# Performance work log

Measured on AMD Instinct MI355X. Metric: run time of the kernel, lower is better.

Reference implementation:

```python
import jax, jax.numpy as jnp
import numpy as np

EPS = 1e-5
DN = ('NCHW', 'OIHW', 'NCHW')

def conv3(x, w):
    return jax.lax.conv_general_dilated(x, w, (1, 1), 'SAME', dimension_numbers=DN)

def conv1(x, w, b):
    # w: [O, I]
    return jnp.einsum('oi,bihw->bohw', w, x) + b[None, :, None, None]

def bn_relu(x, p):
    # p: [4, C] rows = scale, bias, mean, var (eval-mode BatchNorm2d)
    s, b, m, v = p[0], p[1], p[2], p[3]
    y = s[None, :, None, None] * (x - m[None, :, None, None]) * jax.lax.rsqrt(v[None, :, None, None] + EPS) + b[None, :, None, None]
    return jax.nn.relu(y)

def setup_inputs() -> dict:
    key = jax.random.key(0)
    ks = jax.random.split(key, 24)
    B, Cin, H, W = 2, 2048, 60, 60
    Ci = Cin // 4            # 512 inter_channels
    Cq = Ci // 8             # 64  query/key channels
    Co = 40                  # out_channels (classes)
    f32 = jnp.float32
    def bn(C):
        return jnp.stack([jnp.ones((C,), f32), jnp.zeros((C,), f32), jnp.zeros((C,), f32), jnp.ones((C,), f32)])
    s3 = 1.0 / np.sqrt(9 * Ci)
    inp = {
        'x': jax.random.normal(ks[0], (B, Cin, H, W), f32),
        'd': jax.random.uniform(ks[1], (B, 1, H, W), f32),
        'w_s0': jax.random.normal(ks[2], (Ci, Cin, 3, 3), f32) * (1.0 / np.sqrt(9 * Cin)),
        'bn_s0': bn(Ci),
        'wq': jax.random.normal(ks[3], (Cq, Ci), f32) * (1.0 / np.sqrt(Ci)),
        'bq': jnp.zeros((Cq,), f32),
        'wk': jax.random.normal(ks[4], (Cq, Ci), f32) * (1.0 / np.sqrt(Ci)),
        'bk': jnp.zeros((Cq,), f32),
        'wv': jax.random.normal(ks[5], (Ci, Ci), f32) * (1.0 / np.sqrt(Ci)),
        'bv': jnp.zeros((Ci,), f32),
        'gamma_sa': jnp.zeros((), f32) + 0.5,   # nonzero so attention branch contributes
        'lamb': jnp.zeros((), f32) + 0.3,
        'w_s1': jax.random.normal(ks[6], (Ci, Ci, 3, 3), f32) * s3,
        'bn_s1': bn(Ci),
        'w6': jax.random.normal(ks[7], (Co, Ci), f32) * (1.0 / np.sqrt(Ci)),
        'b6': jnp.zeros((Co,), f32),
        'w_c0': jax.random.normal(ks[8], (Ci, Cin, 3, 3), f32) * (1.0 / np.sqrt(9 * Cin)),
        'bn_c0': bn(Ci),
        'gamma_sc': jnp.zeros((), f32) + 0.5,
        'w_c1': jax.random.normal(ks[9], (Ci, Ci, 3, 3), f32) * s3,
        'bn_c1': bn(Ci),
        'w7': jax.random.normal(ks[10], (Co, Ci), f32) * (1.0 / np.sqrt(Ci)),
        'b7': jnp.zeros((Co,), f32),
        'w8': jax.random.normal(ks[11], (Co, Ci), f32) * (1.0 / np.sqrt(Ci)),
        'b8': jnp.zeros((Co,), f32),
    }
    return inp

def reference(x, d, w_s0, bn_s0, wq, bq, wk, bk, wv, bv, gamma_sa, lamb,
              w_s1, bn_s1, w6, b6, w_c0, bn_c0, gamma_sc, w_c1, bn_c1, w7, b7, w8, b8):
    B, _, H, W = x.shape
    N = H * W
    # ---- position-attention (PAM_Module_Dep, fuse_type='a', depth_order=2) branch ----
    feat1 = bn_relu(conv3(x, w_s0), bn_s0)               # [B, Ci, H, W]
    Ci = feat1.shape[1]
    q = conv1(feat1, wq, bq).reshape(B, -1, N)           # [B, Cq, N]
    k = conv1(feat1, wk, bk).reshape(B, -1, N)           # [B, Cq, N]
    v = conv1(feat1, wv, bv).reshape(B, Ci, N)           # [B, Ci, N]
    energy = jnp.einsum('bcn,bcm->bnm', q, k)            # [B, N, N], n=query pixel
    df = d.reshape(B, N)
    dd = (df[:, :, None] - df[:, None, :]) ** 2          # depth_order == 2
    attention = jax.nn.softmax(energy + lamb * dd, axis=-1)
    sa = jnp.einsum('bcm,bnm->bcn', v, attention).reshape(B, Ci, H, W)
    sa = gamma_sa * sa + feat1
    sa_conv = bn_relu(conv3(sa, w_s1), bn_s1)            # post_conv=True
    sa_output = conv1(sa_conv, w6, b6)                   # Dropout2d is identity in eval
    # ---- channel-attention (CAM_Module) branch ----
    feat2 = bn_relu(conv3(x, w_c0), bn_c0)               # [B, Ci, H, W]
    xf = feat2.reshape(B, Ci, N)
    cen = jnp.einsum('bcn,bdn->bcd', xf, xf)             # [B, Ci, Ci]
    cen = jnp.max(cen, axis=-1, keepdims=True) - cen
    catt = jax.nn.softmax(cen, axis=-1)
    sc = jnp.einsum('bcd,bdn->bcn', catt, xf).reshape(B, Ci, H, W)
    sc = gamma_sc * sc + feat2
    sc_conv = bn_relu(conv3(sc, w_c1), bn_c1)
    sc_output = conv1(sc_conv, w7, b7)
    # ---- fusion head ----
    feat_sum = sa_conv + sc_conv
    sasc_output = conv1(feat_sum, w8, b8)
    return (sasc_output, sa_output, sc_output)
```

## Files before the change

kernel.cpp:

```cpp
#include <hip/hip_runtime.h>
#include <stdint.h>

#define DI __device__ __forceinline__

typedef unsigned short u16;
typedef unsigned int u32;
typedef __attribute__((ext_vector_type(8))) short short8;
typedef __attribute__((ext_vector_type(4))) float floatx4;

constexpr int NPIX = 3600;
constexpr int NK   = 3712;
constexpr int PP   = 4096;
constexpr int GUARD= 128;
constexpr int CIN  = 2048, CI = 512, CQ = 64;

constexpr size_t OFF_XPM    = 0;
constexpr size_t OFF_SAF    = 0;
constexpr size_t OFF_PBUF   = 14745600;
constexpr size_t OFF_SACONV = 0;
constexpr size_t OFF_SCCONV = 8388608;
constexpr size_t R1_END     = 42812416;
constexpr size_t OFF_FEAT1  = R1_END;
constexpr size_t OFF_FEAT2  = OFF_FEAT1 + 8388608;
constexpr size_t OFF_SAPM   = OFF_FEAT2 + 8388608;
constexpr size_t OFF_SCPM   = OFF_SAPM + 8912896;
constexpr size_t OFF_W      = OFF_SCPM + 8912896;
constexpr size_t OFF_WQB = OFF_W;
constexpr size_t OFF_WKB = OFF_W + 65536;
constexpr size_t OFF_WVB = OFF_W + 131072;
constexpr size_t OFF_QC  = OFF_W + 655360;
constexpr size_t OFF_KC  = OFF_W + 1576960;
constexpr size_t OFF_VC  = OFF_W + 2498560;
constexpr size_t OFF_WT1 = OFF_W;
constexpr size_t OFF_WT2 = OFF_W + 4718592;
constexpr size_t OFF_VCM = OFF_W + 9871360;
constexpr size_t OFF_CEN = OFF_W + 17473536;
constexpr size_t OFF_CATT= OFF_W + 19570688;
constexpr size_t OFF_WH  = OFF_W + 20619264;
constexpr size_t WS_NEED = OFF_W + 37748736;

DI float b2f(u16 s){ u32 u = ((u32)s)<<16; float f; __builtin_memcpy(&f,&u,4); return f; }
DI u16 f2b(float f){ u32 u; __builtin_memcpy(&u,&f,4); u32 r=(u+0x7fffu+((u>>16)&1u))>>16; return (u16)r; }
DI int pad_of(int n){ int y=n/60, x=n-y*60; return ((y+2)<<6)+x+2; }
DI bool interior(int p){ int py=p>>6, px=p&63; return (py>=2)&&(py<62)&&(px>=2)&&(px<62); }
DI int compact_of(int p){ return ((p>>6)-2)*60 + (p&63) - 2; }
DI void gll16(const void* g, void* l){
  __builtin_amdgcn_global_load_lds((const __attribute__((address_space(1))) void*)g,
                                   (__attribute__((address_space(3))) void*)l, 16, 0, 0);
}
DI float wred_min(float v){
#pragma unroll
  for(int m=32;m;m>>=1) v=fminf(v,__shfl_xor(v,m,64));
  return v;
}
DI float wred_sum(float v){
#pragma unroll
  for(int m=32;m;m>>=1) v+=__shfl_xor(v,m,64);
  return v;
}

struct GArgs {
  const u16 *A, *A2, *B, *B2; u16 *Cb, *Cb2, *Cb3; float* Cf;
  const u16* resid;
  const float *bn, *bn2, *bias, *bias2, *bias3, *gamma, *lambp, *dR, *dC;
  long sA, sB, sC, sres;
  int M, N, KT, ktps, lda, ldb, ldc, Mclamp, Nclamp, nsplit, ksplit, kps;
};

template<int MODE, bool SHIFT, bool NCAT, bool DUALZ, int U, bool SPLITK, bool KCAT2=false>
__global__ __launch_bounds__(256) void k_gemm(GArgs g){
  __shared__ alignas(16) short As[U*4096];
  __shared__ alignas(16) short Bs[U*4096];
  const int bz = blockIdx.z;
  const int sel = DUALZ ? (bz>>1) : 0;
  int bt  = DUALZ ? (bz&1)  : bz;
  int slice = 0;
  if constexpr(SPLITK){ bt = bz / g.ksplit; slice = bz - bt*g.ksplit; }
  const u16* Ab = ((DUALZ && sel) ? g.A2 : g.A) + (long)bt*g.sA;
  const u16* Ab2 = KCAT2 ? (g.A2 + (long)bt*g.sA) : nullptr;
  const u16* Bb = ((DUALZ && sel) ? g.B2 : g.B) + (long)bt*g.sB;
  const int m0 = blockIdx.x*128, n0 = blockIdx.y*128;
  const int tid = threadIdx.x, wid = tid>>6, lane = tid&63;
  const int wr = wid>>1, wc = wid&1;
  const int fr = lane&15, fq = lane>>4;
  const int srow = lane>>2;
  const int swz = ((lane&3) ^ ((lane>>3)&3)) << 3;

  long raB[2], rbB[2];
#pragma unroll
  for(int h=0;h<2;h++){
    long ra = m0 + wid*32 + h*16 + srow;
    if (!SHIFT) ra = (ra > g.Mclamp) ? (long)g.Mclamp : ra;
    raB[h] = ra*(long)g.lda + swz;
    long rb = n0 + wid*32 + h*16 + srow;
    rb = (rb > g.Nclamp) ? (long)g.Nclamp : rb;
    rbB[h] = rb*(long)g.ldb + swz;
  }
  const int ldsOff[2] = { (wid*32)*64, (wid*32+16)*64 };
  const int rswz = (fq ^ ((fr>>1)&3)) << 3;
  const int aRdO = (wr*64+fr)*32 + rswz;
  const int bRdO = (wc*64+fr)*32 + rswz;

  floatx4 acc[4][4];
#pragma unroll
  for(int i=0;i<4;i++)
#pragma unroll
    for(int j=0;j<4;j++)
#pragma unroll
      for(int e=0;e<4;e++) acc[i][j][e]=0.f;

  if constexpr(SHIFT){
    const int KB = g.ktps;
    for(int s=0; s<9; ++s){
      const long aoff = (long)((s/3)*64 + (s-(s/3)*3) - 65)*g.lda;
      const long boff = (long)s*KB*32;
      for(int kb=0; kb<KB; kb+=U){
        __syncthreads();
#pragma unroll
        for(int u=0;u<U;++u){
          const int ko = (kb+u)*32;
#pragma unroll
          for(int h=0;h<2;h++){
            gll16(Ab + raB[h] + aoff + ko, (char*)As + u*8192 + ldsOff[h]);
            gll16(Bb + rbB[h] + boff + ko, (char*)Bs + u*8192 + ldsOff[h]);
          }
        }
        __syncthreads();
#pragma unroll
        for(int u=0;u<U;++u){
          short8 af[4], bfv[4];
#pragma unroll
          for(int mi=0;mi<4;mi++) af[mi]  = *(const short8*)(As + u*4096 + aRdO + mi*512);
#pragma unroll
          for(int ni=0;ni<4;ni++) bfv[ni] = *(const short8*)(Bs + u*4096 + bRdO + ni*512);
#pragma unroll
          for(int mi=0;mi<4;mi++)
#pragma unroll
            for(int ni=0;ni<4;ni++)
              acc[mi][ni] = __builtin_amdgcn_mfma_f32_16x16x32_bf16(af[mi], bfv[ni], acc[mi][ni], 0,0,0);
        }
      }
    }
  } else {
    int kt0 = 0, ktN = g.KT;
    if constexpr(SPLITK){ kt0 = slice*g.kps; ktN = min(g.KT, kt0+g.kps); }
    for(int kt=kt0; kt<ktN; kt+=U){
      __syncthreads();
#pragma unroll
      for(int u=0;u<U;++u){
        if (kt+u < ktN){
          int ko = kt+u;
          const u16* srcA = Ab;
          if constexpr(KCAT2){ if (ko >= (g.KT>>1)){ srcA = Ab2; ko -= (g.KT>>1); } }
          const int koB = (kt+u)*32;
#pragma unroll
          for(int h=0;h<2;h++){
            gll16(srcA + raB[h] + ko*32, (char*)As + u*8192 + ldsOff[h]);
            gll16(Bb + rbB[h] + koB, (char*)Bs + u*8192 + ldsOff[h]);
          }
        }
      }
      __syncthreads();
#pragma unroll
      for(int u=0;u<U;++u){
        if (kt+u < ktN){
          short8 af[4], bfv[4];
#pragma unroll
          for(int mi=0;mi<4;mi++) af[mi]  = *(const short8*)(As + u*4096 + aRdO + mi*512);
#pragma unroll
          for(int ni=0;ni<4;ni++) bfv[ni] = *(const short8*)(Bs + u*4096 + bRdO + ni*512);
#pragma unroll
          for(int mi=0;mi<4;mi++)
#pragma unroll
            for(int ni=0;ni<4;ni++)
              acc[mi][ni] = __builtin_amdgcn_mfma_f32_16x16x32_bf16(af[mi], bfv[ni], acc[mi][ni], 0,0,0);
        }
      }
    }
  }

  float* Cf = (MODE==3) ? g.Cf + (long)bt*g.sC : nullptr;
  const u16* Rb = (MODE==5) ? g.resid + (long)bt*g.sres : nullptr;
  float gamv=0.f;
  if constexpr(MODE==5) gamv = *g.gamma;

#pragma unroll
  for(int ni=0;ni<4;ni++){
    const int gc = n0 + wc*64 + ni*16 + fr;
    if (gc >= g.N) continue;
    if constexpr(MODE==0){
      const float* bnP = g.bn; u16* CbP = g.Cb; int oc = gc;
      if constexpr(DUALZ){ if (sel){ bnP = g.bn2; CbP = g.Cb2; } }
      if constexpr(NCAT){ if (gc >= g.nsplit){ bnP = g.bn2; CbP = g.Cb2; oc = gc - g.nsplit; } }
      CbP += (long)bt*g.sC;
      const float s_=bnP[oc], bb=bnP[CI+oc], mm=bnP[2*CI+oc], vv=bnP[3*CI+oc];
      const float cA = s_*rsqrtf(vv+1e-5f), cB = bb - cA*mm;
#pragma unroll
      for(int mi=0;mi<4;mi++)
#pragma unroll
        for(int j=0;j<4;j++){
          const int gr = m0 + wr*64 + mi*16 + fq*4 + j;
          if (interior(gr)) CbP[(size_t)gr*g.ldc + oc] = f2b(fmaxf(cA*acc[mi][ni][j]+cB, 0.f));
        }
    } else if constexpr(MODE==6){
      u16* dst; int col, ld; float bs;
      if (gc < 64){ dst = g.Cb  + (long)bt*((long)NPIX*CQ); col=gc;     ld=CQ; bs=g.bias[gc]; }
      else if (gc < 128){ dst = g.Cb2 + (long)bt*((long)NPIX*CQ); col=gc-64; ld=CQ; bs=g.bias2[gc-64]; }
      else { dst = g.Cb3 + (long)bt*((long)NPIX*CI); col=gc-128; ld=CI; bs=g.bias3[gc-128]; }
#pragma unroll
      for(int mi=0;mi<4;mi++)
#pragma unroll
        for(int j=0;j<4;j++){
          const int gr = m0 + wr*64 + mi*16 + fq*4 + j;
          if (interior(gr)) dst[(size_t)compact_of(gr)*ld + col] = f2b(acc[mi][ni][j] + bs);
        }
    } else if constexpr(MODE==3){
#pragma unroll
      for(int mi=0;mi<4;mi++)
#pragma unroll
        for(int j=0;j<4;j++){
          const int gr = m0 + wr*64 + mi*16 + fq*4 + j;
          if (gr < g.M){
            if constexpr(SPLITK) atomicAdd(&Cf[(size_t)gr*g.ldc + gc], acc[mi][ni][j]);
            else Cf[(size_t)gr*g.ldc + gc] = acc[mi][ni][j];
          }
        }
    } else if constexpr(MODE==5){
      u16* CbP = g.Cb + (long)bt*g.sC;
#pragma unroll
      for(int mi=0;mi<4;mi++)
#pragma unroll
        for(int j=0;j<4;j++){
          const int gr = m0 + wr*64 + mi*16 + fq*4 + j;
          if (interior(gr)){ const size_t o=(size_t)gr*g.ldc + gc; CbP[o] = f2b(gamv*acc[mi][ni][j] + b2f(Rb[o])); }
        }
    } else if constexpr(MODE==7){
      size_t hb; int oc; const float* bp;
      if (gc < 40){ hb = 0; oc = gc; bp = g.bias; }
      else if (gc < 80){ hb = 288000; oc = gc-40; bp = g.bias2; }
      else { hb = 576000; oc = gc-80; bp = g.bias3; }
      float* dst = g.Cf + hb + (size_t)bt*144000 + (size_t)oc*3600;
      const float bsv = bp[oc];
#pragma unroll
      for(int mi=0;mi<4;mi++)
#pragma unroll
        for(int j=0;j<4;j++){
          const int gr = m0 + wr*64 + mi*16 + fq*4 + j;
          if (interior(gr)) dst[compact_of(gr)] = acc[mi][ni][j] + bsv;
        }
    }
  }
}

__global__ __launch_bounds__(512) void k_esm(const u16* __restrict__ qc, const u16* __restrict__ kc,
    const float* __restrict__ dd, const float* __restrict__ lamp, u16* __restrict__ pb){
  __shared__ float lm[8][16], ll[8][16];
  const int tid = threadIdx.x, wave = tid>>6, lane = tid&63;
  const int fr = lane&15, fq = lane>>4;
  const int q0 = blockIdx.x*16;
  const float lam = *lamp;
  const u16* qp = qc + (size_t)(q0+fr)*CQ + fq*8;
  const short8 qa0 = *(const short8*)(qp);
  const short8 qa1 = *(const short8*)(qp + 32);
  float dr[4];
#pragma unroll
  for(int j=0;j<4;j++) dr[j] = dd[q0 + fq*4 + j];
  float m[4], l[4];
#pragma unroll
  for(int j=0;j<4;j++){ m[j] = -3e38f; l[j] = 0.f; }

  for(int t=wave; t<29; t+=8){
    const int n0 = t*128;
    floatx4 s[8]; float dc[8];
#pragma unroll
    for(int ni=0; ni<8; ++ni){
      const int ccol = min(n0 + ni*16 + fr, NPIX-1);
      const u16* kp = kc + (size_t)ccol*CQ + fq*8;
      const short8 b0 = *(const short8*)(kp);
      const short8 b1 = *(const short8*)(kp + 32);
      floatx4 z = {0.f,0.f,0.f,0.f};
      z = __builtin_amdgcn_mfma_f32_16x16x32_bf16(qa0, b0, z, 0,0,0);
      s[ni] = __builtin_amdgcn_mfma_f32_16x16x32_bf16(qa1, b1, z, 0,0,0);
      dc[ni] = dd[ccol];
    }
#pragma unroll
    for(int j=0;j<4;j++){
      float vals[8]; float tmax = -3e38f;
#pragma unroll
      for(int ni=0;ni<8;ni++){
        const float td = dr[j] - dc[ni];
        float v = s[ni][j] + lam*td*td;
        if (n0 + ni*16 + fr >= NPIX) v = -3e38f;
        vals[ni] = v; tmax = fmaxf(tmax, v);
      }
      tmax = fmaxf(tmax, __shfl_xor(tmax,1,64));
      tmax = fmaxf(tmax, __shfl_xor(tmax,2,64));
      tmax = fmaxf(tmax, __shfl_xor(tmax,4,64));
      tmax = fmaxf(tmax, __shfl_xor(tmax,8,64));
      const float mn = fmaxf(m[j], tmax);
      float ts = 0.f;
#pragma unroll
      for(int ni=0;ni<8;ni++) ts += __expf(vals[ni]-mn);
      ts += __shfl_xor(ts,1,64);
      ts += __shfl_xor(ts,2,64);
      ts += __shfl_xor(ts,4,64);
      ts += __shfl_xor(ts,8,64);
      l[j] = l[j]*__expf(m[j]-mn) + ts;
      m[j] = mn;
    }
  }
  if (fr == 0){
#pragma unroll
    for(int j=0;j<4;j++){ lm[wave][fq*4+j] = m[j]; ll[wave][fq*4+j] = l[j]; }
  }
  __syncthreads();
  float M[4], L[4];
#pragma unroll
  for(int j=0;j<4;j++){
    const int row = fq*4 + j;
    float mm = lm[0][row];
#pragma unroll
    for(int w=1;w<8;w++) mm = fmaxf(mm, lm[w][row]);
    float ss = 0.f;
#pragma unroll
    for(int w=0;w<8;w++) ss += ll[w][row]*__expf(lm[w][row]-mm);
    M[j] = mm; L[j] = 1.f/ss;
  }

  for(int t=wave; t<29; t+=8){
    const int n0 = t*128;
#pragma unroll
    for(int ni=0; ni<8; ++ni){
      const int col = n0 + ni*16 + fr;
      const int ccol = min(col, NPIX-1);
      const u16* kp = kc + (size_t)ccol*CQ + fq*8;
      const short8 b0 = *(const short8*)(kp);
      const short8 b1 = *(const short8*)(kp + 32);
      floatx4 z = {0.f,0.f,0.f,0.f};
      z = __builtin_amdgcn_mfma_f32_16x16x32_bf16(qa0, b0, z, 0,0,0);
      const floatx4 sv = __builtin_amdgcn_mfma_f32_16x16x32_bf16(qa1, b1, z, 0,0,0);
      const float dcv = dd[ccol];
#pragma unroll
      for(int j=0;j<4;j++){
        const int q = q0 + fq*4 + j;
        const float td = dr[j] - dcv;
        float v = sv[j] + lam*td*td;
        if (col >= NPIX) v = -3e38f;
        const float p = __expf(v - M[j])*L[j];
        pb[(size_t)q*NK + col] = f2b(p);
      }
    }
  }
}

__global__ __launch_bounds__(256) void k_padx(const float* __restrict__ x, u16* __restrict__ xpm){
  __shared__ alignas(16) u16 t[64][72];
  const int n0 = blockIdx.x*64, c0 = blockIdx.y*64, b = blockIdx.z;
  const float* xb = x + (size_t)b*CIN*NPIX;
  u16* ob = xpm + (size_t)b*(PP+2*GUARD)*CIN + (size_t)GUARD*CIN;
  const int tid = threadIdx.x;
#pragma unroll
  for(int pass=0; pass<2; ++pass){
    const int cl = pass*32 + (tid>>3);
    const int nn = (tid&7)*8;
    const int n = n0 + nn;
    const float* src = xb + (size_t)(c0+cl)*NPIX + n;
    u16 r[8];
    if (n + 7 < NPIX){
      const float4 v0 = *(const float4*)src;
      const float4 v1 = *(const float4*)(src+4);
      r[0]=f2b(v0.x); r[1]=f2b(v0.y); r[2]=f2b(v0.z); r[3]=f2b(v0.w);
      r[4]=f2b(v1.x); r[5]=f2b(v1.y); r[6]=f2b(v1.z); r[7]=f2b(v1.w);
    } else {
#pragma unroll
      for(int j=0;j<8;j++){ const int nj=n+j; r[j] = (nj<NPIX)? f2b(src[j]) : (u16)0; }
    }
    __builtin_memcpy(&t[cl][nn], r, 16);
  }
  __syncthreads();
#pragma unroll
  for(int pass=0; pass<2; ++pass){
    const int nl = pass*32 + (tid>>3);
    const int cc = (tid&7)*8;
    const int n = n0 + nl;
    if (n < NPIX){
      u16 v[8];
#pragma unroll
      for(int j=0;j<8;j++) v[j] = t[cc+j][nl];
      uint4 vv; __builtin_memcpy(&vv, v, 16);
      *(uint4*)(ob + (size_t)pad_of(n)*CIN + c0 + cc) = vv;
    }
  }
}

template<bool PADIN>
__global__ __launch_bounds__(256) void k_to_cm(const u16* __restrict__ in, u16* __restrict__ out,
                                               long sIn, long sOut){
  __shared__ alignas(16) u16 t[64][72];
  const int n0 = blockIdx.x*64, c0 = blockIdx.y*64, b = blockIdx.z;
  const u16* ib = in + (size_t)b*sIn;
  u16* ob = out + (size_t)b*sOut;
  const int tid = threadIdx.x;
#pragma unroll
  for(int pass=0; pass<2; ++pass){
    const int nl = pass*32 + (tid>>3);
    const int cc = (tid&7)*8;
    const int n = n0 + nl;
    uint4 v = {0,0,0,0};
    if (n < NPIX){
      const int r = PADIN ? pad_of(n) : n;
      v = *(const uint4*)(ib + (size_t)r*CI + c0 + cc);
    }
    *(uint4*)&t[nl][cc] = v;
  }
  __syncthreads();
#pragma unroll
  for(int pass=0; pass<2; ++pass){
    const int cl = pass*32 + (tid>>3);
    const int nn = (tid&7)*8;
    const int n = n0 + nn;
    if (n < NK){
      u16 v[8];
#pragma unroll
      for(int j=0;j<8;j++) v[j] = t[nn+j][cl];
      uint4 vv; __builtin_memcpy(&vv, v, 16);
      *(uint4*)(ob + (size_t)(c0+cl)*NK + n) = vv;
    }
  }
}

__global__ __launch_bounds__(256) void k_wt(const float* __restrict__ w, u16* __restrict__ wt, int Kc){
  const int idx = blockIdx.x*256 + threadIdx.x;
  const int o = idx / Kc, i = idx - o*Kc;
  u16 v[9];
#pragma unroll
  for(int s=0;s<9;s++) v[s] = f2b(w[(size_t)idx*9 + s]);
#pragma unroll
  for(int s=0;s<9;s++) wt[(size_t)o*9*Kc + (size_t)s*Kc + i] = v[s];
}

__global__ __launch_bounds__(256) void k_cvt(const float* __restrict__ src, u16* __restrict__ dst, int n){
  const int i = blockIdx.x*256 + threadIdx.x;
  if (i < n) dst[i] = f2b(src[i]);
}

__global__ __launch_bounds__(256) void k_whead(const float* __restrict__ w6, const float* __restrict__ w7,
                                               const float* __restrict__ w8, u16* __restrict__ wh){
  const int idx = blockIdx.x*256 + threadIdx.x;
  const int r = idx >> 10, k = idx & 1023;
  float v = 0.f;
  if (r < 40) v = w8[r*512 + (k & 511)];
  else if (r < 80){ if (k < 512) v = w6[(r-40)*512 + k]; }
  else { if (k >= 512) v = w7[(r-80)*512 + (k-512)]; }
  wh[idx] = f2b(v);
}

__global__ __launch_bounds__(256) void k_csoftmax(const float* __restrict__ cen, u16* __restrict__ catt){
  const int c = blockIdx.x, b = blockIdx.y, tid = threadIdx.x;
  const float* e = cen + ((size_t)b*CI + c)*CI;
  u16* o = catt + ((size_t)b*CI + c)*CI;
  __shared__ float red[8];
  const float a0 = e[tid], a1 = e[tid+256];
  float lmin = fminf(a0,a1);
  lmin = wred_min(lmin);
  if((tid&63)==0) red[tid>>6]=lmin;
  __syncthreads();
  const float m0 = fminf(fminf(red[0],red[1]),fminf(red[2],red[3]));
  const float x0 = __expf(m0-a0), x1 = __expf(m0-a1);
  float ls = x0+x1;
  ls = wred_sum(ls);
  if((tid&63)==0) red[4+(tid>>6)]=ls;
  __syncthreads();
  const float inv = 1.f/(red[4]+red[5]+red[6]+red[7]);
  o[tid] = f2b(x0*inv); o[tid+256] = f2b(x1*inv);
}

__global__ __launch_bounds__(256) void k_pv_ep(const float* __restrict__ saf, const u16* __restrict__ f1,
                                               u16* __restrict__ sapm, const float* __restrict__ gamma){
  const int idx = blockIdx.x*256 + threadIdx.x;
  const int n = idx >> 6, c = (idx & 63) * 8;
  const float gam = *gamma;
  const int p = pad_of(n);
  const float4 v0 = *(const float4*)(saf + (size_t)n*CI + c);
  const float4 v1 = *(const float4*)(saf + (size_t)n*CI + c + 4);
  const uint4 rv = *(const uint4*)(f1 + (size_t)p*CI + c);
  const u16* rp = (const u16*)&rv;
  u16 o[8];
  o[0]=f2b(gam*v0.x + b2f(rp[0])); o[1]=f2b(gam*v0.y + b2f(rp[1]));
  o[2]=f2b(gam*v0.z + b2f(rp[2])); o[3]=f2b(gam*v0.w + b2f(rp[3]));
  o[4]=f2b(gam*v1.x + b2f(rp[4])); o[5]=f2b(gam*v1.y + b2f(rp[5]));
  o[6]=f2b(gam*v1.z + b2f(rp[6])); o[7]=f2b(gam*v1.w + b2f(rp[7]));
  uint4 ov; __builtin_memcpy(&ov, o, 16);
  *(uint4*)(sapm + (size_t)p*CI + c) = ov;
}

extern "C" void kernel_launch(void* const* d_in, const int* in_sizes, int n_in,
                              void* d_out, int out_size, void* d_ws, size_t ws_size,
                              hipStream_t stream){
  (void)in_sizes; (void)n_in; (void)out_size;
  if (ws_size < WS_NEED) return;

  const float* x    = (const float*)d_in[0];
  const float* dd   = (const float*)d_in[1];
  const float* w_s0 = (const float*)d_in[2];
  const float* bn_s0= (const float*)d_in[3];
  const float* wq   = (const float*)d_in[4];
  const float* bq   = (const float*)d_in[5];
  const float* wk   = (const float*)d_in[6];
  const float* bk   = (const float*)d_in[7];
  const float* wv   = (const float*)d_in[8];
  const float* bv   = (const float*)d_in[9];
  const float* gsa  = (const float*)d_in[10];
  const float* lam  = (const float*)d_in[11];
  const float* w_s1 = (const float*)d_in[12];
  const float* bn_s1= (const float*)d_in[13];
  const float* w6   = (const float*)d_in[14];
  const float* b6   = (const float*)d_in[15];
  const float* w_c0 = (const float*)d_in[16];
  const float* bn_c0= (const float*)d_in[17];
  const float* gsc  = (const float*)d_in[18];
  const float* w_c1 = (const float*)d_in[19];
  const float* bn_c1= (const float*)d_in[20];
  const float* w7   = (const float*)d_in[21];
  const float* b7   = (const float*)d_in[22];
  const float* w8   = (const float*)d_in[23];
  const float* b8   = (const float*)d_in[24];

  char* W = (char*)d_ws;
  u16*   XPM   = (u16*)(W + OFF_XPM);
  float* SAF   = (float*)(W + OFF_SAF);
  u16*   PB    = (u16*)(W + OFF_PBUF);
  u16*   SACONV= (u16*)(W + OFF_SACONV);
  u16*   SCCONV= (u16*)(W + OFF_SCCONV);
  u16*   F1    = (u16*)(W + OFF_FEAT1);
  u16*   F2    = (u16*)(W + OFF_FEAT2);
  u16*   SAPM  = (u16*)(W + OFF_SAPM);
  u16*   SCPM  = (u16*)(W + OFF_SCPM);
  u16*   WTT   = (u16*)(W + OFF_W);
  u16*   WQB   = (u16*)(W + OFF_WQB);
  u16*   WKB   = (u16*)(W + OFF_WKB);
  u16*   WVB   = (u16*)(W + OFF_WVB);
  u16*   QC    = (u16*)(W + OFF_QC);
  u16*   KC    = (u16*)(W + OFF_KC);
  u16*   VC    = (u16*)(W + OFF_VC);
  u16*   WT1   = (u16*)(W + OFF_WT1);
  u16*   WT2   = (u16*)(W + OFF_WT2);
  u16*   WH    = (u16*)(W + OFF_WH);
  u16*   VCM   = (u16*)(W + OFF_VCM);
  u16*   F2CM  = VCM;
  float* CEN   = (float*)(W + OFF_CEN);
  u16*   CATT  = (u16*)(W + OFF_CATT);
  float* OUT   = (float*)d_out;

  hipMemsetAsync(XPM,  0, (size_t)2*(PP+2*GUARD)*CIN*2, stream);
  hipMemsetAsync(SAPM, 0, (size_t)2*(PP+2*GUARD)*CI*2,  stream);
  hipMemsetAsync(SCPM, 0, (size_t)2*(PP+2*GUARD)*CI*2,  stream);

  k_padx<<<dim3(57,32,2),256,0,stream>>>(x, XPM);

  k_wt<<<(512*2048)/256,256,0,stream>>>(w_s0, WTT, 2048);
  k_wt<<<(512*2048)/256,256,0,stream>>>(w_c0, WTT + (size_t)512*9*2048, 2048);
  GArgs a{};
  a.A = XPM + (size_t)GUARD*CIN; a.B = WTT; a.Cb = F1; a.Cb2 = F2;
  a.bn = bn_s0; a.bn2 = bn_c0;
  a.sA = (long)(PP+2*GUARD)*CIN; a.sB = 0; a.sC = (long)PP*CI;
  a.M = PP; a.N = 1024; a.nsplit = 512; a.KT = 576; a.ktps = 64;
  a.lda = CIN; a.ldb = 9*2048; a.ldc = CI; a.Mclamp = PP-1; a.Nclamp = 1023;
  k_gemm<0,true,true,false,4,false><<<dim3(32,8,2),256,0,stream>>>(a);

  k_cvt<<<(64*512+255)/256,256,0,stream>>>(wq, WQB, 64*512);
  k_cvt<<<(64*512+255)/256,256,0,stream>>>(wk, WKB, 64*512);
  k_cvt<<<(512*512+255)/256,256,0,stream>>>(wv, WVB, 512*512);

  GArgs q{};
  q.A = F1; q.sA = (long)PP*CI; q.lda = CI;
  q.M = PP; q.Mclamp = PP-1; q.KT = 16; q.ktps = 16;
  q.B = WQB; q.sB = 0; q.ldb = CI; q.N = 640; q.Nclamp = 639;
  q.Cb = QC; q.Cb2 = KC; q.Cb3 = VC; q.bias = bq; q.bias2 = bk; q.bias3 = bv;
  k_gemm<6,false,false,false,4,false><<<dim3(32,5,2),256,0,stream>>>(q);

  k_to_cm<false><<<dim3(NK/64, CI/64, 2),256,0,stream>>>(VC, VCM, (long)NPIX*CI, (long)CI*NK);

  for(int bb=0; bb<2; ++bb){
    k_esm<<<dim3(225),512,0,stream>>>(QC + (size_t)bb*NPIX*CQ, KC + (size_t)bb*NPIX*CQ,
                                      dd + (size_t)bb*NPIX, lam, PB);
    hipMemsetAsync(SAF, 0, (size_t)NPIX*CI*4, stream);
    GArgs p{};
    p.A = PB; p.B = VCM + (size_t)bb*CI*NK;
    p.Cf = SAF;
    p.M = NPIX; p.N = CI; p.KT = NK/32; p.ktps = NK/32;
    p.lda = NK; p.ldb = NK; p.ldc = CI; p.sC = 0;
    p.Mclamp = NPIX-1; p.Nclamp = CI-1;
    p.ksplit = 2; p.kps = NK/64;
    k_gemm<3,false,false,false,4,true><<<dim3(29, 4, 2),256,0,stream>>>(p);
    k_pv_ep<<<dim3(NPIX*CI/8/256),256,0,stream>>>(SAF, F1 + (size_t)bb*PP*CI,
                                                  SAPM + (size_t)bb*(PP+2*GUARD)*CI + (size_t)GUARD*CI, gsa);
  }

  k_to_cm<true><<<dim3(NK/64, CI/64, 2),256,0,stream>>>(F2, F2CM, (long)PP*CI, (long)CI*NK);
  hipMemsetAsync(CEN, 0, (size_t)2*CI*CI*4, stream);
  GArgs c{};
  c.A = F2CM; c.B = F2CM; c.Cf = CEN;
  c.sA = (long)CI*NK; c.sB = (long)CI*NK; c.sC = (long)CI*CI;
  c.M = CI; c.N = CI; c.KT = NK/32; c.ktps = NK/32;
  c.lda = NK; c.ldb = NK; c.ldc = CI; c.Mclamp = CI-1; c.Nclamp = CI-1;
  c.ksplit = 8; c.kps = (NK/32 + 7)/8;
  k_gemm<3,false,false,false,1,true><<<dim3(4, 4, 16),256,0,stream>>>(c);
  k_csoftmax<<<dim3(CI,2),256,0,stream>>>(CEN, CATT);
  GArgs s{};
  s.A = F2; s.B = CATT;
  s.Cb = SCPM + (size_t)GUARD*CI;
  s.resid = F2; s.gamma = gsc;
  s.sA = (long)PP*CI; s.sB = (long)CI*CI; s.sC = (long)(PP+2*GUARD)*CI; s.sres = (long)PP*CI;
  s.M = PP; s.N = CI; s.KT = 16; s.ktps = 16;
  s.lda = CI; s.ldb = CI; s.ldc = CI; s.Mclamp = PP-1; s.Nclamp = CI-1;
  k_gemm<5,false,false,false,4,false><<<dim3(32, 4, 2),256,0,stream>>>(s);

  k_wt<<<(512*512)/256,256,0,stream>>>(w_s1, WT1, 512);
  k_wt<<<(512*512)/256,256,0,stream>>>(w_c1, WT2, 512);
  k_whead<<<dim3(120*1024/256),256,0,stream>>>(w6, w7, w8, WH);
  GArgs t{};
  t.A = SAPM + (size_t)GUARD*CI; t.A2 = SCPM + (size_t)GUARD*CI;
  t.B = WT1; t.B2 = WT2;
  t.Cb = SACONV; t.Cb2 = SCCONV; t.bn = bn_s1; t.bn2 = bn_c1;
  t.sA = (long)(PP+2*GUARD)*CI; t.sB = 0; t.sC = (long)PP*CI;
  t.M = PP; t.N = CI; t.KT = 144; t.ktps = 16;
  t.lda = CI; t.ldb = 9*512; t.ldc = CI; t.Mclamp = PP-1; t.Nclamp = CI-1;
  k_gemm<0,true,false,true,4,false><<<dim3(32,4,4),256,0,stream>>>(t);

  GArgs h{};
  h.A = SACONV; h.A2 = SCCONV; h.B = WH; h.Cf = OUT;
  h.bias = b8; h.bias2 = b6; h.bias3 = b7;
  h.sA = (long)PP*CI; h.sB = 0; h.sC = 0;
  h.M = PP; h.N = 120; h.KT = 32; h.ktps = 32;
  h.lda = CI; h.ldb = 1024; h.ldc = 0; h.Mclamp = PP-1; h.Nclamp = 119;
  k_gemm<7,false,false,false,4,false,true><<<dim3(32,1,2),256,0,stream>>>(h);
}
```

Measured before the change: 752.9 us.

## Skip padded border tiles, zero only halo rows, merge weight-conversion launches

```diff
diff --git a/kernel.cpp b/kernel.cpp
--- a/kernel.cpp
+++ b/kernel.cpp
@@ -64,7 +64,7 @@
   const u16* resid;
   const float *bn, *bn2, *bias, *bias2, *bias3, *gamma, *lambp, *dR, *dC;
   long sA, sB, sC, sres;
-  int M, N, KT, ktps, lda, ldb, ldc, Mclamp, Nclamp, nsplit, ksplit, kps;
+  int M, N, KT, ktps, lda, ldb, ldc, Mclamp, Nclamp, nsplit, ksplit, kps, moff;
 };
 
 template<int MODE, bool SHIFT, bool NCAT, bool DUALZ, int U, bool SPLITK, bool KCAT2=false>
@@ -79,7 +79,7 @@
   const u16* Ab = ((DUALZ && sel) ? g.A2 : g.A) + (long)bt*g.sA;
   const u16* Ab2 = KCAT2 ? (g.A2 + (long)bt*g.sA) : nullptr;
   const u16* Bb = ((DUALZ && sel) ? g.B2 : g.B) + (long)bt*g.sB;
-  const int m0 = blockIdx.x*128, n0 = blockIdx.y*128;
+  const int m0 = blockIdx.x*128 + g.moff, n0 = blockIdx.y*128;
   const int tid = threadIdx.x, wid = tid>>6, lane = tid&63;
   const int wr = wid>>1, wc = wid&1;
   const int fr = lane&15, fq = lane>>4;
@@ -353,6 +353,19 @@
   }
 }
 
+__global__ __launch_bounds__(256) void k_zring(u16* __restrict__ base, int C, long slabStride){
+  const int row = blockIdx.x, slab = blockIdx.y;
+  bool z;
+  if (row < GUARD || row >= GUARD+PP) z = true;
+  else z = !interior(row - GUARD);
+  if (!z) return;
+  u16* p = base + (size_t)slab*slabStride + (size_t)row*C;
+  for (int i = threadIdx.x*8; i < C; i += 256*8){
+    uint4 zz = {0,0,0,0};
+    *(uint4*)(p + i) = zz;
+  }
+}
+
 __global__ __launch_bounds__(256) void k_padx(const float* __restrict__ x, u16* __restrict__ xpm){
   __shared__ alignas(16) u16 t[64][72];
   const int n0 = blockIdx.x*64, c0 = blockIdx.y*64, b = blockIdx.z;
@@ -429,7 +442,10 @@
   }
 }
 
-__global__ __launch_bounds__(256) void k_wt(const float* __restrict__ w, u16* __restrict__ wt, int Kc){
+__global__ __launch_bounds__(256) void k_wt2(const float* __restrict__ wA, const float* __restrict__ wB,
+                                             u16* __restrict__ wtA, u16* __restrict__ wtB, int Kc){
+  const float* w = blockIdx.y ? wB : wA;
+  u16* wt = blockIdx.y ? wtB : wtA;
   const int idx = blockIdx.x*256 + threadIdx.x;
   const int o = idx / Kc, i = idx - o*Kc;
   u16 v[9];
@@ -439,9 +455,17 @@
   for(int s=0;s<9;s++) wt[(size_t)o*9*Kc + (size_t)s*Kc + i] = v[s];
 }
 
-__global__ __launch_bounds__(256) void k_cvt(const float* __restrict__ src, u16* __restrict__ dst, int n){
+__global__ __launch_bounds__(256) void k_cvt3(const float* __restrict__ a, int na,
+                                              const float* __restrict__ b, int nb,
+                                              const float* __restrict__ c, int nc,
+                                              u16* __restrict__ dst){
   const int i = blockIdx.x*256 + threadIdx.x;
-  if (i < n) dst[i] = f2b(src[i]);
+  float v;
+  if (i < na) v = a[i];
+  else if (i < na+nb) v = b[i-na];
+  else if (i < na+nb+nc) v = c[i-na-nb];
+  else return;
+  dst[i] = f2b(v);
 }
 
 __global__ __launch_bounds__(256) void k_whead(const float* __restrict__ w6, const float* __restrict__ w7,
@@ -538,8 +562,6 @@
   u16*   SCPM  = (u16*)(W + OFF_SCPM);
   u16*   WTT   = (u16*)(W + OFF_W);
   u16*   WQB   = (u16*)(W + OFF_WQB);
-  u16*   WKB   = (u16*)(W + OFF_WKB);
-  u16*   WVB   = (u16*)(W + OFF_WVB);
   u16*   QC    = (u16*)(W + OFF_QC);
   u16*   KC    = (u16*)(W + OFF_KC);
   u16*   VC    = (u16*)(W + OFF_VC);
@@ -552,32 +574,28 @@
   u16*   CATT  = (u16*)(W + OFF_CATT);
   float* OUT   = (float*)d_out;
 
-  hipMemsetAsync(XPM,  0, (size_t)2*(PP+2*GUARD)*CIN*2, stream);
-  hipMemsetAsync(SAPM, 0, (size_t)2*(PP+2*GUARD)*CI*2,  stream);
-  hipMemsetAsync(SCPM, 0, (size_t)2*(PP+2*GUARD)*CI*2,  stream);
+  k_zring<<<dim3(PP+2*GUARD, 2),256,0,stream>>>(XPM,  CIN, (long)(PP+2*GUARD)*CIN);
+  k_zring<<<dim3(PP+2*GUARD, 4),256,0,stream>>>(SAPM, CI,  (long)(PP+2*GUARD)*CI);
 
   k_padx<<<dim3(57,32,2),256,0,stream>>>(x, XPM);
 
-  k_wt<<<(512*2048)/256,256,0,stream>>>(w_s0, WTT, 2048);
-  k_wt<<<(512*2048)/256,256,0,stream>>>(w_c0, WTT + (size_t)512*9*2048, 2048);
+  k_wt2<<<dim3((512*2048)/256, 2),256,0,stream>>>(w_s0, w_c0, WTT, WTT + (size_t)512*9*2048, 2048);
   GArgs a{};
   a.A = XPM + (size_t)GUARD*CIN; a.B = WTT; a.Cb = F1; a.Cb2 = F2;
   a.bn = bn_s0; a.bn2 = bn_c0;
   a.sA = (long)(PP+2*GUARD)*CIN; a.sB = 0; a.sC = (long)PP*CI;
   a.M = PP; a.N = 1024; a.nsplit = 512; a.KT = 576; a.ktps = 64;
-  a.lda = CIN; a.ldb = 9*2048; a.ldc = CI; a.Mclamp = PP-1; a.Nclamp = 1023;
-  k_gemm<0,true,true,false,4,false><<<dim3(32,8,2),256,0,stream>>>(a);
-
-  k_cvt<<<(64*512+255)/256,256,0,stream>>>(wq, WQB, 64*512);
-  k_cvt<<<(64*512+255)/256,256,0,stream>>>(wk, WKB, 64*512);
-  k_cvt<<<(512*512+255)/256,256,0,stream>>>(wv, WVB, 512*512);
+  a.lda = CIN; a.ldb = 9*2048; a.ldc = CI; a.Mclamp = PP-1; a.Nclamp = 1023; a.moff = 128;
+  k_gemm<0,true,true,false,4,false><<<dim3(30,8,2),256,0,stream>>>(a);
+
+  k_cvt3<<<dim3((64*512+64*512+512*512)/256),256,0,stream>>>(wq, 64*512, wk, 64*512, wv, 512*512, WQB);
 
   GArgs q{};
   q.A = F1; q.sA = (long)PP*CI; q.lda = CI;
-  q.M = PP; q.Mclamp = PP-1; q.KT = 16; q.ktps = 16;
+  q.M = PP; q.Mclamp = PP-1; q.KT = 16; q.ktps = 16; q.moff = 128;
   q.B = WQB; q.sB = 0; q.ldb = CI; q.N = 640; q.Nclamp = 639;
   q.Cb = QC; q.Cb2 = KC; q.Cb3 = VC; q.bias = bq; q.bias2 = bk; q.bias3 = bv;
-  k_gemm<6,false,false,false,4,false><<<dim3(32,5,2),256,0,stream>>>(q);
+  k_gemm<6,false,false,false,4,false><<<dim3(30,5,2),256,0,stream>>>(q);
 
   k_to_cm<false><<<dim3(NK/64, CI/64, 2),256,0,stream>>>(VC, VCM, (long)NPIX*CI, (long)CI*NK);
 
@@ -591,8 +609,8 @@
     p.M = NPIX; p.N = CI; p.KT = NK/32; p.ktps = NK/32;
     p.lda = NK; p.ldb = NK; p.ldc = CI; p.sC = 0;
     p.Mclamp = NPIX-1; p.Nclamp = CI-1;
-    p.ksplit = 2; p.kps = NK/64;
-    k_gemm<3,false,false,false,4,true><<<dim3(29, 4, 2),256,0,stream>>>(p);
+    p.ksplit = 4; p.kps = NK/128;
+    k_gemm<3,false,false,false,4,true><<<dim3(29, 4, 4),256,0,stream>>>(p);
     k_pv_ep<<<dim3(NPIX*CI/8/256),256,0,stream>>>(SAF, F1 + (size_t)bb*PP*CI,
                                                   SAPM + (size_t)bb*(PP+2*GUARD)*CI + (size_t)GUARD*CI, gsa);
   }
@@ -612,27 +630,26 @@
   s.Cb = SCPM + (size_t)GUARD*CI;
   s.resid = F2; s.gamma = gsc;
   s.sA = (long)PP*CI; s.sB = (long)CI*CI; s.sC = (long)(PP+2*GUARD)*CI; s.sres = (long)PP*CI;
-  s.M = PP; s.N = CI; s.KT = 16; s.ktps = 16;
+  s.M = PP; s.N = CI; s.KT = 16; s.ktps = 16; s.moff = 128;
   s.lda = CI; s.ldb = CI; s.ldc = CI; s.Mclamp = PP-1; s.Nclamp = CI-1;
-  k_gemm<5,false,false,false,4,false><<<dim3(32, 4, 2),256,0,stream>>>(s);
-
-  k_wt<<<(512*512)/256,256,0,stream>>>(w_s1, WT1, 512);
-  k_wt<<<(512*512)/256,256,0,stream>>>(w_c1, WT2, 512);
+  k_gemm<5,false,false,false,4,false><<<dim3(30, 4, 2),256,0,stream>>>(s);
+
+  k_wt2<<<dim3((512*512)/256, 2),256,0,stream>>>(w_s1, w_c1, WT1, WT2, 512);
   k_whead<<<dim3(120*1024/256),256,0,stream>>>(w6, w7, w8, WH);
   GArgs t{};
   t.A = SAPM + (size_t)GUARD*CI; t.A2 = SCPM + (size_t)GUARD*CI;
   t.B = WT1; t.B2 = WT2;
   t.Cb = SACONV; t.Cb2 = SCCONV; t.bn = bn_s1; t.bn2 = bn_c1;
   t.sA = (long)(PP+2*GUARD)*CI; t.sB = 0; t.sC = (long)PP*CI;
-  t.M = PP; t.N = CI; t.KT = 144; t.ktps = 16;
+  t.M = PP; t.N = CI; t.KT = 144; t.ktps = 16; t.moff = 128;
   t.lda = CI; t.ldb = 9*512; t.ldc = CI; t.Mclamp = PP-1; t.Nclamp = CI-1;
-  k_gemm<0,true,false,true,4,false><<<dim3(32,4,4),256,0,stream>>>(t);
+  k_gemm<0,true,false,true,4,false><<<dim3(30,4,4),256,0,stream>>>(t);
 
   GArgs h{};
   h.A = SACONV; h.A2 = SCCONV; h.B = WH; h.Cf = OUT;
   h.bias = b8; h.bias2 = b6; h.bias3 = b7;
   h.sA = (long)PP*CI; h.sB = 0; h.sC = 0;
-  h.M = PP; h.N = 120; h.KT = 32; h.ktps = 32;
+  h.M = PP; h.N = 120; h.KT = 32; h.ktps = 32; h.moff = 128;
   h.lda = CI; h.ldb = 1024; h.ldc = 0; h.Mclamp = PP-1; h.Nclamp = 119;
-  k_gemm<7,false,false,false,4,false,true><<<dim3(32,1,2),256,0,stream>>>(h);
-}
+  k_gemm<7,false,false,false,4,false,true><<<dim3(30,1,2),256,0,stream>>>(h);
+}
```

Measured after the change: 853.0 us. 13.3% more time.
